# Kernel tuning notes

Measured on AMD Instinct MI355X. Metric: run time of the kernel, lower is better.

## Reference

```python
import jax, jax.numpy as jnp
import numpy as np

GAMMA = 5.0 / 3.0
N, H = 131072, 256


def mlp(c, W1, b1, W2, b2, W3, b3, W4, b4):
    h = jnp.tanh(c @ W1 + b1)
    h = jnp.tanh(h @ W2 + b2)
    h = jnp.tanh(h @ W3 + b3)
    return h @ W4 + b4  # [N, 6] -> (rho, vx, vy, Bx, By, P)


def setup_inputs() -> dict:
    key = jax.random.key(0)
    ks = jax.random.split(key, 6)
    s = 0.5
    return {
        "coords": jax.random.uniform(ks[0], (N, 3), jnp.float32),  # (x, y, t)
        "W1": jax.random.normal(ks[1], (3, H), jnp.float32) * s,
        "b1": jnp.zeros((H,), jnp.float32),
        "W2": jax.random.normal(ks[2], (H, H), jnp.float32) * (s / np.sqrt(H)),
        "b2": jnp.zeros((H,), jnp.float32),
        "W3": jax.random.normal(ks[3], (H, H), jnp.float32) * (s / np.sqrt(H)),
        "b3": jnp.zeros((H,), jnp.float32),
        "W4": jax.random.normal(ks[4], (H, 6), jnp.float32) * (s / np.sqrt(H)),
        "b4": jnp.zeros((6,), jnp.float32),
        "weights": jnp.ones((7,), jnp.float32),
    }


def reference(coords, W1, b1, W2, b2, W3, b3, W4, b4, weights):
    f = lambda c: mlp(c, W1, b1, W2, b2, W3, b3, W4, b4)
    preds = f(coords)
    # Batched Jacobian d preds / d coords via 3 forward-mode JVPs (basis dirs x,y,t)
    eye = jnp.eye(3, dtype=coords.dtype)
    jvp1 = lambda e: jax.jvp(f, (coords,), (jnp.broadcast_to(e, coords.shape),))[1]
    J = jnp.transpose(jax.vmap(jvp1)(eye), (1, 2, 0))  # [N, 6, 3]

    rho, vx, vy, Bx, By, P = (preds[:, k] for k in range(6))
    Jx, Jy, Jt = J[..., 0], J[..., 1], J[..., 2]  # each [N, 6]

    # time derivatives (chain rule for composite fields)
    dt_rho = Jt[:, 0]
    dt_Bx, dt_By = Jt[:, 3], Jt[:, 4]
    dt_rhovx = dt_rho * vx + rho * Jt[:, 1]
    dt_rhovy = dt_rho * vy + rho * Jt[:, 2]

    def dE(Jc):  # derivative of total energy E along coord c
        return (Jc[:, 5] / (GAMMA - 1.0)
                + 0.5 * Jc[:, 0] * (vx ** 2 + vy ** 2)
                + rho * (vx * Jc[:, 1] + vy * Jc[:, 2])
                + Bx * Jc[:, 3] + By * Jc[:, 4])

    dE_dx, dE_dy, dE_dt = dE(Jx), dE(Jy), dE(Jt)

    div_v = Jx[:, 1] + Jy[:, 2]
    div_B = Jx[:, 3] + Jy[:, 4]
    continuity = dt_rho + rho * div_v

    # grad of total pressure P + 0.5*(Bx^2 + By^2)
    dPm_dx = Jx[:, 5] + Bx * Jx[:, 3] + By * Jx[:, 4]
    dPm_dy = Jy[:, 5] + Bx * Jy[:, 3] + By * Jy[:, 4]
    momentum_x = dt_rhovx + dPm_dx - (Bx * Jx[:, 3] + By * Jy[:, 3])
    momentum_y = dt_rhovy + dPm_dy - (Bx * Jx[:, 4] + By * Jy[:, 4])

    # induction: G = vx*By - vy*Bx
    def dG(Jc):
        return Jc[:, 1] * By + vx * Jc[:, 4] - Jc[:, 2] * Bx - vy * Jc[:, 3]

    induction_x = dt_Bx + dG(Jy)
    induction_y = dt_By - dG(Jx)

    # energy: d/dt E + div( S*v - D*B ), S = E + P + Pm, D = B.v
    E = P / (GAMMA - 1.0) + 0.5 * rho * (vx ** 2 + vy ** 2) + 0.5 * (Bx ** 2 + By ** 2)
    S = E + P + 0.5 * (Bx ** 2 + By ** 2)
    dS_dx = dE_dx + Jx[:, 5] + Bx * Jx[:, 3] + By * Jx[:, 4]
    dS_dy = dE_dy + Jy[:, 5] + Bx * Jy[:, 3] + By * Jy[:, 4]
    D = Bx * vx + By * vy

    def dD(Jc):
        return Jc[:, 3] * vx + Bx * Jc[:, 1] + Jc[:, 4] * vy + By * Jc[:, 2]

    dFx_dx = dS_dx * vx + S * Jx[:, 1] - dD(Jx) * Bx - D * Jx[:, 3]
    dFy_dy = dS_dy * vy + S * Jy[:, 2] - dD(Jy) * By - D * Jy[:, 4]
    energy = dE_dt + dFx_dx + dFy_dy

    res = [continuity, momentum_x, momentum_y, induction_x, induction_y, energy, div_B]
    loss = sum(w * jnp.mean(r ** 2) for w, r in zip(weights, res))
    return loss
```

## Files before the change

kernel.cpp:

```cpp
#include <hip/hip_runtime.h>
#include <hip/hip_bf16.h>
#include <cstdint>


#define LDW 264
#define TPTS 16
#define GRIDB 256

typedef __attribute__((ext_vector_type(8))) short v8h;
typedef __attribute__((ext_vector_type(4))) float v4f;

__device__ __forceinline__ ushort f2b(float f) {
    uint32_t u = __float_as_uint(f);
    u = (u + 0x7fffu + ((u >> 16) & 1u)) >> 16;
    return (ushort)u;
}
__device__ __forceinline__ uint32_t pk2(float a, float b) {
    union { __hip_bfloat162 h2; uint32_t u; } cv;
    cv.h2 = __float22bfloat162_rn(make_float2(a, b));
    return cv.u;
}
__device__ __forceinline__ float fast_tanh(float x) {
    float e = __expf(2.0f * x);
    return 1.0f - 2.0f * __builtin_amdgcn_rcpf(e + 1.0f);
}

__global__ void prep_weights(const float* __restrict__ W2, const float* __restrict__ W3,
                             const float* __restrict__ W4,
                             ushort* __restrict__ Wt2, ushort* __restrict__ Wt3,
                             ushort* __restrict__ Wt4) {
    int idx = blockIdx.x * 256 + threadIdx.x;
    if (idx < 65536) {
        int k = idx >> 8, n = idx & 255;
        Wt2[n * 256 + k] = f2b(W2[k * 256 + n]);
        Wt3[n * 256 + k] = f2b(W3[k * 256 + n]);
    }
    if (idx < 4096) {
        int n = idx >> 8, k = idx & 255;
        Wt4[n * 256 + k] = (n < 6) ? f2b(W4[k * 6 + n]) : (ushort)0;
    }
}

__device__ __forceinline__ void dense_layer(const ushort* __restrict__ src,
                                            ushort* __restrict__ dst,
                                            const v8h (*wf)[8], const v4f* bs,
                                            int wv, int q, int l15) {
    v4f acc[2][4];
    #pragma unroll
    for (int a = 0; a < 2; a++)
        #pragma unroll
        for (int b = 0; b < 4; b++) {
            v4f z = {0.0f, 0.0f, 0.0f, 0.0f};
            acc[a][b] = z;
        }
    #pragma unroll
    for (int kk = 0; kk < 8; kk++) {
        v8h B[4];
        #pragma unroll
        for (int nt = 0; nt < 4; nt++)
            B[nt] = *(const v8h*)(&src[(nt * 16 + l15) * LDW + kk * 32 + q * 8]);
        #pragma unroll
        for (int mt = 0; mt < 2; mt++)
            #pragma unroll
            for (int nt = 0; nt < 4; nt++)
                acc[mt][nt] = __builtin_amdgcn_mfma_f32_16x16x32_bf16(wf[mt][kk], B[nt], acc[mt][nt], 0, 0, 0);
    }
    #pragma unroll
    for (int mt = 0; mt < 2; mt++) {
        const int colb = wv * 32 + mt * 16 + q * 4;
        v4f bb = bs[mt];
        float h0 = fast_tanh(acc[mt][0][0] + bb[0]);
        float h1 = fast_tanh(acc[mt][0][1] + bb[1]);
        float h2 = fast_tanh(acc[mt][0][2] + bb[2]);
        float h3 = fast_tanh(acc[mt][0][3] + bb[3]);
        float d0 = 1.0f - h0 * h0, d1 = 1.0f - h1 * h1;
        float d2 = 1.0f - h2 * h2, d3 = 1.0f - h3 * h3;
        uint2 w;
        w.x = pk2(h0, h1); w.y = pk2(h2, h3);
        *(uint2*)(&dst[l15 * LDW + colb]) = w;
        #pragma unroll
        for (int s = 1; s < 4; s++) {
            w.x = pk2(d0 * acc[mt][s][0], d1 * acc[mt][s][1]);
            w.y = pk2(d2 * acc[mt][s][2], d3 * acc[mt][s][3]);
            *(uint2*)(&dst[(s * 16 + l15) * LDW + colb]) = w;
        }
    }
}

__global__ __launch_bounds__(512, 2)
void mhd_fused(const float* __restrict__ coords,
               const float* __restrict__ W1, const float* __restrict__ b1,
               const float* __restrict__ b2, const float* __restrict__ b3,
               const float* __restrict__ b4,
               const float* __restrict__ wts,
               const ushort* __restrict__ Wt2, const ushort* __restrict__ Wt3,
               const ushort* __restrict__ Wt4,
               float* __restrict__ out, int npts, float inv_n) {
    __shared__ ushort Xs0[64 * LDW];
    __shared__ ushort Xs1[64 * LDW];
    __shared__ ushort W4s[16 * LDW];
    __shared__ float  cs[TPTS * 3];
    __shared__ float  Y4[4][TPTS][8];

    const int tid  = threadIdx.x;
    const int lane = tid & 63;
    const int wv   = tid >> 6;
    const int q    = lane >> 4;
    const int l15  = lane & 15;

    for (int idx = tid; idx < 16 * 256; idx += 512)
        W4s[(idx >> 8) * LDW + (idx & 255)] = Wt4[idx];

    v8h w2f[2][8], w3f[2][8];
    v4f bs2[2], bs3[2];
    #pragma unroll
    for (int mt = 0; mt < 2; mt++) {
        const int nrow = (wv * 32 + mt * 16 + l15) * 256 + q * 8;
        #pragma unroll
        for (int kk = 0; kk < 8; kk++) {
            w2f[mt][kk] = *(const v8h*)(&Wt2[nrow + kk * 32]);
            w3f[mt][kk] = *(const v8h*)(&Wt3[nrow + kk * 32]);
        }
        bs2[mt] = *(const v4f*)(&b2[wv * 32 + mt * 16 + q * 4]);
        bs3[mt] = *(const v4f*)(&b3[wv * 32 + mt * 16 + q * 4]);
    }

    const int jj = tid & 255, ph = tid >> 8;
    const float l1w0 = W1[jj], l1w1 = W1[256 + jj], l1w2 = W1[512 + jj], l1b = b1[jj];
    const float b40 = b4[0], b41 = b4[1], b42 = b4[2], b43 = b4[3], b44 = b4[4], b45 = b4[5];
    const float wt0 = wts[0], wt1 = wts[1], wt2_ = wts[2], wt3_ = wts[3],
                wt4_ = wts[4], wt5 = wts[5], wt6 = wts[6];

    const int ntiles = (npts + TPTS - 1) / TPTS;
    float vsum = 0.0f;

    for (int tile = blockIdx.x; tile < ntiles; tile += GRIDB) {
        const int base = tile * TPTS;

        if (tid < TPTS * 3) {
            int p = tid / 3, c = tid % 3;
            int gp = base + p; if (gp >= npts) gp = npts - 1;
            cs[tid] = coords[gp * 3 + c];
        }
        __syncthreads();

        #pragma unroll
        for (int pp = 0; pp < 8; pp++) {
            const int p = ph * 8 + pp;
            float x = cs[p * 3], y = cs[p * 3 + 1], t = cs[p * 3 + 2];
            float pre = fmaf(x, l1w0, fmaf(y, l1w1, fmaf(t, l1w2, l1b)));
            float h = fast_tanh(pre);
            float d = 1.0f - h * h;
            Xs0[p * LDW + jj]        = f2b(h);
            Xs0[(16 + p) * LDW + jj] = f2b(d * l1w0);
            Xs0[(32 + p) * LDW + jj] = f2b(d * l1w1);
            Xs0[(48 + p) * LDW + jj] = f2b(d * l1w2);
        }
        __syncthreads();

        dense_layer(Xs0, Xs1, w2f, bs2, wv, q, l15);
        __syncthreads();
        dense_layer(Xs1, Xs0, w3f, bs3, wv, q, l15);
        __syncthreads();

        if (wv < 4) {
            v4f a4 = {0.0f, 0.0f, 0.0f, 0.0f};
            #pragma unroll
            for (int kk = 0; kk < 8; kk++) {
                v8h A = *(const v8h*)(&W4s[l15 * LDW + kk * 32 + q * 8]);
                v8h B = *(const v8h*)(&Xs0[(wv * 16 + l15) * LDW + kk * 32 + q * 8]);
                a4 = __builtin_amdgcn_mfma_f32_16x16x32_bf16(A, B, a4, 0, 0, 0);
            }
            if (q < 2) {
                #pragma unroll
                for (int r = 0; r < 4; r++)
                    Y4[wv][l15][q * 4 + r] = a4[r];
            }
        }
        __syncthreads();

        if (tid < 16 && (base + tid) < npts) {
            const float* Yh = Y4[0][tid];
            const float* JX = Y4[1][tid];
            const float* JY = Y4[2][tid];
            const float* JT = Y4[3][tid];
            const float g1 = 1.5f;
            float rho = Yh[0] + b40, vx = Yh[1] + b41, vy = Yh[2] + b42;
            float Bx  = Yh[3] + b43, By = Yh[4] + b44, P  = Yh[5] + b45;
            float v2 = vx * vx + vy * vy;
            float dt_rho = JT[0];
            float dt_rhovx = dt_rho * vx + rho * JT[1];
            float dt_rhovy = dt_rho * vy + rho * JT[2];
            auto dE = [&](const float* J) {
                return J[5] * g1 + 0.5f * J[0] * v2 + rho * (vx * J[1] + vy * J[2]) + Bx * J[3] + By * J[4];
            };
            float dE_dx = dE(JX), dE_dy = dE(JY), dE_dt = dE(JT);
            float div_v = JX[1] + JY[2];
            float div_B = JX[3] + JY[4];
            float continuity = dt_rho + rho * div_v;
            float dPm_dx = JX[5] + Bx * JX[3] + By * JX[4];
            float dPm_dy = JY[5] + Bx * JY[3] + By * JY[4];
            float momentum_x = dt_rhovx + dPm_dx - (Bx * JX[3] + By * JY[3]);
            float momentum_y = dt_rhovy + dPm_dy - (Bx * JX[4] + By * JY[4]);
            auto dG = [&](const float* J) {
                return J[1] * By + vx * J[4] - J[2] * Bx - vy * J[3];
            };
            float induction_x = JT[3] + dG(JY);
            float induction_y = JT[4] - dG(JX);
            float E = P * g1 + 0.5f * rho * v2 + 0.5f * (Bx * Bx + By * By);
            float S = E + P + 0.5f * (Bx * Bx + By * By);
            float dS_dx = dE_dx + JX[5] + Bx * JX[3] + By * JX[4];
            float dS_dy = dE_dy + JY[5] + Bx * JY[3] + By * JY[4];
            float D = Bx * vx + By * vy;
            auto dD = [&](const float* J) {
                return J[3] * vx + Bx * J[1] + J[4] * vy + By * J[2];
            };
            float dFx_dx = dS_dx * vx + S * JX[1] - dD(JX) * Bx - D * JX[3];
            float dFy_dy = dS_dy * vy + S * JY[2] - dD(JY) * By - D * JY[4];
            float energy = dE_dt + dFx_dx + dFy_dy;
            vsum += wt0 * continuity * continuity
                  + wt1 * momentum_x * momentum_x
                  + wt2_ * momentum_y * momentum_y
                  + wt3_ * induction_x * induction_x
                  + wt4_ * induction_y * induction_y
                  + wt5 * energy * energy
                  + wt6 * div_B * div_B;
        }
    }

    if (tid < 64) {
        #pragma unroll
        for (int off = 8; off >= 1; off >>= 1)
            vsum += __shfl_down(vsum, off, 64);
        if (tid == 0) atomicAdd(out, vsum * inv_n);
    }
}

extern "C" void kernel_launch(void* const* d_in, const int* in_sizes, int n_in,
                              void* d_out, int out_size, void* d_ws, size_t ws_size,
                              hipStream_t stream) {
    const float* coords = (const float*)d_in[0];
    const float* W1 = (const float*)d_in[1];
    const float* b1 = (const float*)d_in[2];
    const float* W2 = (const float*)d_in[3];
    const float* b2 = (const float*)d_in[4];
    const float* W3 = (const float*)d_in[5];
    const float* b3 = (const float*)d_in[6];
    const float* W4 = (const float*)d_in[7];
    const float* b4 = (const float*)d_in[8];
    const float* wts = (const float*)d_in[9];
    const int npts = in_sizes[0] / 3;

    ushort* Wt2 = (ushort*)d_ws;
    ushort* Wt3 = Wt2 + 65536;
    ushort* Wt4 = Wt3 + 65536;

    hipMemsetAsync(d_out, 0, sizeof(float), stream);
    prep_weights<<<256, 256, 0, stream>>>(W2, W3, W4, Wt2, Wt3, Wt4);
    mhd_fused<<<GRIDB, 512, 0, stream>>>(coords, W1, b1, b2, b3, b4, wts,
                                         Wt2, Wt3, Wt4, (float*)d_out, npts, 1.0f / npts);
}
```

Measured before the change: 247.8 us.

## Software-pipeline layer-1 and residual across tiles with XOR-swizzled LDS

Replaces the padded LDS layout with an XOR-swizzled 512-byte row layout to avoid bank conflicts, and double-buffers the layer-1 input so the next tile's first layer is computed before the current tile's dense layers. The residual evaluation is deferred by two iterations into a double-buffered Y4, run by wave 7 while other work proceeds, which drops one barrier per tile. Layer 1 now reads coords directly from global memory and writes 4 columns per thread as vector stores. LDS use grows (an extra input buffer), which may limit occupancy at two blocks per CU.

Result: slower. 322.1 us (+30.0%).

```diff
diff --git a/kernel.cpp b/kernel.cpp
--- a/kernel.cpp
+++ b/kernel.cpp
@@ -3,9 +3,8 @@
 #include <cstdint>
 
 
-#define LDW 264
+#define GRIDB 256
 #define TPTS 16
-#define GRIDB 256
 
 typedef __attribute__((ext_vector_type(8))) short v8h;
 typedef __attribute__((ext_vector_type(4))) float v4f;
@@ -23,6 +22,9 @@
 __device__ __forceinline__ float fast_tanh(float x) {
     float e = __expf(2.0f * x);
     return 1.0f - 2.0f * __builtin_amdgcn_rcpf(e + 1.0f);
+}
+__device__ __forceinline__ int swz(int row, int bytecol) {
+    return (row << 9) + ((((bytecol >> 4) ^ (row & 31)) << 4) | (bytecol & 15));
 }
 
 __global__ void prep_weights(const float* __restrict__ W2, const float* __restrict__ W3,
@@ -41,52 +43,6 @@
     }
 }
 
-__device__ __forceinline__ void dense_layer(const ushort* __restrict__ src,
-                                            ushort* __restrict__ dst,
-                                            const v8h (*wf)[8], const v4f* bs,
-                                            int wv, int q, int l15) {
-    v4f acc[2][4];
-    #pragma unroll
-    for (int a = 0; a < 2; a++)
-        #pragma unroll
-        for (int b = 0; b < 4; b++) {
-            v4f z = {0.0f, 0.0f, 0.0f, 0.0f};
-            acc[a][b] = z;
-        }
-    #pragma unroll
-    for (int kk = 0; kk < 8; kk++) {
-        v8h B[4];
-        #pragma unroll
-        for (int nt = 0; nt < 4; nt++)
-            B[nt] = *(const v8h*)(&src[(nt * 16 + l15) * LDW + kk * 32 + q * 8]);
-        #pragma unroll
-        for (int mt = 0; mt < 2; mt++)
-            #pragma unroll
-            for (int nt = 0; nt < 4; nt++)
-                acc[mt][nt] = __builtin_amdgcn_mfma_f32_16x16x32_bf16(wf[mt][kk], B[nt], acc[mt][nt], 0, 0, 0);
-    }
-    #pragma unroll
-    for (int mt = 0; mt < 2; mt++) {
-        const int colb = wv * 32 + mt * 16 + q * 4;
-        v4f bb = bs[mt];
-        float h0 = fast_tanh(acc[mt][0][0] + bb[0]);
-        float h1 = fast_tanh(acc[mt][0][1] + bb[1]);
-        float h2 = fast_tanh(acc[mt][0][2] + bb[2]);
-        float h3 = fast_tanh(acc[mt][0][3] + bb[3]);
-        float d0 = 1.0f - h0 * h0, d1 = 1.0f - h1 * h1;
-        float d2 = 1.0f - h2 * h2, d3 = 1.0f - h3 * h3;
-        uint2 w;
-        w.x = pk2(h0, h1); w.y = pk2(h2, h3);
-        *(uint2*)(&dst[l15 * LDW + colb]) = w;
-        #pragma unroll
-        for (int s = 1; s < 4; s++) {
-            w.x = pk2(d0 * acc[mt][s][0], d1 * acc[mt][s][1]);
-            w.y = pk2(d2 * acc[mt][s][2], d3 * acc[mt][s][3]);
-            *(uint2*)(&dst[(s * 16 + l15) * LDW + colb]) = w;
-        }
-    }
-}
-
 __global__ __launch_bounds__(512, 2)
 void mhd_fused(const float* __restrict__ coords,
                const float* __restrict__ W1, const float* __restrict__ b1,
@@ -96,11 +52,11 @@
                const ushort* __restrict__ Wt2, const ushort* __restrict__ Wt3,
                const ushort* __restrict__ Wt4,
                float* __restrict__ out, int npts, float inv_n) {
-    __shared__ ushort Xs0[64 * LDW];
-    __shared__ ushort Xs1[64 * LDW];
-    __shared__ ushort W4s[16 * LDW];
-    __shared__ float  cs[TPTS * 3];
-    __shared__ float  Y4[4][TPTS][8];
+    __shared__ __align__(16) uint8_t XinB[2][64 * 512];
+    __shared__ __align__(16) uint8_t Xmid[64 * 512];
+    __shared__ __align__(16) uint8_t Xout[64 * 512];
+    __shared__ __align__(16) uint8_t W4s[16 * 512];
+    __shared__ float Y4[2][4][TPTS][8];
 
     const int tid  = threadIdx.x;
     const int lane = tid & 63;
@@ -108,8 +64,11 @@
     const int q    = lane >> 4;
     const int l15  = lane & 15;
 
-    for (int idx = tid; idx < 16 * 256; idx += 512)
-        W4s[(idx >> 8) * LDW + (idx & 255)] = Wt4[idx];
+    for (int idx = tid; idx < 16 * 128; idx += 512) {
+        int n = idx >> 7, kdw = idx & 127;
+        *(uint32_t*)(&W4s[(n << 9) + ((((kdw >> 2) ^ n) << 4) | ((kdw & 3) << 2))]) =
+            ((const uint32_t*)Wt4)[idx];
+    }
 
     v8h w2f[2][8], w3f[2][8];
     v4f bs2[2], bs3[2];
@@ -125,114 +84,184 @@
         bs3[mt] = *(const v4f*)(&b3[wv * 32 + mt * 16 + q * 4]);
     }
 
-    const int jj = tid & 255, ph = tid >> 8;
-    const float l1w0 = W1[jj], l1w1 = W1[256 + jj], l1w2 = W1[512 + jj], l1b = b1[jj];
+    const int j0 = (tid & 63) * 4, pg = tid >> 6;
+    float l1w0[4], l1w1[4], l1w2[4], l1b[4];
+    #pragma unroll
+    for (int c = 0; c < 4; c++) {
+        l1w0[c] = W1[j0 + c]; l1w1[c] = W1[256 + j0 + c];
+        l1w2[c] = W1[512 + j0 + c]; l1b[c] = b1[j0 + c];
+    }
+
     const float b40 = b4[0], b41 = b4[1], b42 = b4[2], b43 = b4[3], b44 = b4[4], b45 = b4[5];
     const float wt0 = wts[0], wt1 = wts[1], wt2_ = wts[2], wt3_ = wts[3],
                 wt4_ = wts[4], wt5 = wts[5], wt6 = wts[6];
 
+    auto do_l1 = [&](int tile, uint8_t* Xin) {
+        const int base = tile * TPTS;
+        #pragma unroll
+        for (int pp = 0; pp < 2; pp++) {
+            const int p = pg * 2 + pp;
+            int gp = base + p; if (gp >= npts) gp = npts - 1;
+            float x = coords[gp * 3], y = coords[gp * 3 + 1], t = coords[gp * 3 + 2];
+            float h[4], d[4];
+            #pragma unroll
+            for (int c = 0; c < 4; c++) {
+                h[c] = fast_tanh(fmaf(x, l1w0[c], fmaf(y, l1w1[c], fmaf(t, l1w2[c], l1b[c]))));
+                d[c] = 1.0f - h[c] * h[c];
+            }
+            uint2 w;
+            const int bc = j0 * 2;
+            w.x = pk2(h[0], h[1]); w.y = pk2(h[2], h[3]);
+            *(uint2*)(&Xin[swz(p, bc)]) = w;
+            w.x = pk2(d[0] * l1w0[0], d[1] * l1w0[1]); w.y = pk2(d[2] * l1w0[2], d[3] * l1w0[3]);
+            *(uint2*)(&Xin[swz(16 + p, bc)]) = w;
+            w.x = pk2(d[0] * l1w1[0], d[1] * l1w1[1]); w.y = pk2(d[2] * l1w1[2], d[3] * l1w1[3]);
+            *(uint2*)(&Xin[swz(32 + p, bc)]) = w;
+            w.x = pk2(d[0] * l1w2[0], d[1] * l1w2[1]); w.y = pk2(d[2] * l1w2[2], d[3] * l1w2[3]);
+            *(uint2*)(&Xin[swz(48 + p, bc)]) = w;
+        }
+    };
+
+    auto dense = [&](const uint8_t* src, uint8_t* dst, const v8h (*wf)[8], const v4f* bs) {
+        v4f acc[2][4];
+        #pragma unroll
+        for (int a = 0; a < 2; a++)
+            #pragma unroll
+            for (int b = 0; b < 4; b++) {
+                v4f z = {0.0f, 0.0f, 0.0f, 0.0f};
+                acc[a][b] = z;
+            }
+        #pragma unroll
+        for (int kk = 0; kk < 8; kk++) {
+            v8h B[4];
+            #pragma unroll
+            for (int nt = 0; nt < 4; nt++) {
+                const int row = nt * 16 + l15;
+                B[nt] = *(const v8h*)(&src[(row << 9) + ((((kk * 4 + q) ^ (row & 31)) << 4))]);
+            }
+            #pragma unroll
+            for (int mt = 0; mt < 2; mt++)
+                #pragma unroll
+                for (int nt = 0; nt < 4; nt++)
+                    acc[mt][nt] = __builtin_amdgcn_mfma_f32_16x16x32_bf16(wf[mt][kk], B[nt], acc[mt][nt], 0, 0, 0);
+        }
+        #pragma unroll
+        for (int mt = 0; mt < 2; mt++) {
+            const int bc = wv * 64 + mt * 32 + q * 8;
+            v4f bb = bs[mt];
+            float h0 = fast_tanh(acc[mt][0][0] + bb[0]);
+            float h1 = fast_tanh(acc[mt][0][1] + bb[1]);
+            float h2 = fast_tanh(acc[mt][0][2] + bb[2]);
+            float h3 = fast_tanh(acc[mt][0][3] + bb[3]);
+            float d0 = 1.0f - h0 * h0, d1 = 1.0f - h1 * h1;
+            float d2 = 1.0f - h2 * h2, d3 = 1.0f - h3 * h3;
+            uint2 w;
+            w.x = pk2(h0, h1); w.y = pk2(h2, h3);
+            *(uint2*)(&dst[swz(l15, bc)]) = w;
+            #pragma unroll
+            for (int s = 1; s < 4; s++) {
+                w.x = pk2(d0 * acc[mt][s][0], d1 * acc[mt][s][1]);
+                w.y = pk2(d2 * acc[mt][s][2], d3 * acc[mt][s][3]);
+                *(uint2*)(&dst[swz(s * 16 + l15, bc)]) = w;
+            }
+        }
+    };
+
+    auto residual = [&](int tile, int par) -> float {
+        const int gp = tile * TPTS + lane;
+        if (gp >= npts) return 0.0f;
+        const float* Yh = Y4[par][0][lane];
+        const float* JX = Y4[par][1][lane];
+        const float* JY = Y4[par][2][lane];
+        const float* JT = Y4[par][3][lane];
+        const float g1 = 1.5f;
+        float rho = Yh[0] + b40, vx = Yh[1] + b41, vy = Yh[2] + b42;
+        float Bx  = Yh[3] + b43, By = Yh[4] + b44, P  = Yh[5] + b45;
+        float v2 = vx * vx + vy * vy;
+        float dt_rho = JT[0];
+        float dt_rhovx = dt_rho * vx + rho * JT[1];
+        float dt_rhovy = dt_rho * vy + rho * JT[2];
+        auto dE = [&](const float* J) {
+            return J[5] * g1 + 0.5f * J[0] * v2 + rho * (vx * J[1] + vy * J[2]) + Bx * J[3] + By * J[4];
+        };
+        float dE_dx = dE(JX), dE_dy = dE(JY), dE_dt = dE(JT);
+        float div_v = JX[1] + JY[2];
+        float div_B = JX[3] + JY[4];
+        float continuity = dt_rho + rho * div_v;
+        float dPm_dx = JX[5] + Bx * JX[3] + By * JX[4];
+        float dPm_dy = JY[5] + Bx * JY[3] + By * JY[4];
+        float momentum_x = dt_rhovx + dPm_dx - (Bx * JX[3] + By * JY[3]);
+        float momentum_y = dt_rhovy + dPm_dy - (Bx * JX[4] + By * JY[4]);
+        auto dG = [&](const float* J) {
+            return J[1] * By + vx * J[4] - J[2] * Bx - vy * J[3];
+        };
+        float induction_x = JT[3] + dG(JY);
+        float induction_y = JT[4] - dG(JX);
+        float E = P * g1 + 0.5f * rho * v2 + 0.5f * (Bx * Bx + By * By);
+        float S = E + P + 0.5f * (Bx * Bx + By * By);
+        float dS_dx = dE_dx + JX[5] + Bx * JX[3] + By * JX[4];
+        float dS_dy = dE_dy + JY[5] + Bx * JY[3] + By * JY[4];
+        float D = Bx * vx + By * vy;
+        auto dD = [&](const float* J) {
+            return J[3] * vx + Bx * J[1] + J[4] * vy + By * J[2];
+        };
+        float dFx_dx = dS_dx * vx + S * JX[1] - dD(JX) * Bx - D * JX[3];
+        float dFy_dy = dS_dy * vy + S * JY[2] - dD(JY) * By - D * JY[4];
+        float energy = dE_dt + dFx_dx + dFy_dy;
+        return wt0 * continuity * continuity
+             + wt1 * momentum_x * momentum_x
+             + wt2_ * momentum_y * momentum_y
+             + wt3_ * induction_x * induction_x
+             + wt4_ * induction_y * induction_y
+             + wt5 * energy * energy
+             + wt6 * div_B * div_B;
+    };
+
     const int ntiles = (npts + TPTS - 1) / TPTS;
+    const int myblk  = blockIdx.x;
+    const int nit    = (myblk < ntiles) ? ((ntiles - 1 - myblk) / GRIDB + 1) : 0;
     float vsum = 0.0f;
 
-    for (int tile = blockIdx.x; tile < ntiles; tile += GRIDB) {
-        const int base = tile * TPTS;
-
-        if (tid < TPTS * 3) {
-            int p = tid / 3, c = tid % 3;
-            int gp = base + p; if (gp >= npts) gp = npts - 1;
-            cs[tid] = coords[gp * 3 + c];
-        }
+    if (nit > 0) do_l1(myblk, XinB[0]);
+
+    for (int i = 0; i < nit; i++) {
+        const int tile = myblk + i * GRIDB;
+        if (wv == 7 && lane < TPTS && i >= 2)
+            vsum += residual(tile - 2 * GRIDB, i & 1);
+        if (i + 1 < nit) do_l1(tile + GRIDB, XinB[(i + 1) & 1]);
         __syncthreads();
-
-        #pragma unroll
-        for (int pp = 0; pp < 8; pp++) {
-            const int p = ph * 8 + pp;
-            float x = cs[p * 3], y = cs[p * 3 + 1], t = cs[p * 3 + 2];
-            float pre = fmaf(x, l1w0, fmaf(y, l1w1, fmaf(t, l1w2, l1b)));
-            float h = fast_tanh(pre);
-            float d = 1.0f - h * h;
-            Xs0[p * LDW + jj]        = f2b(h);
-            Xs0[(16 + p) * LDW + jj] = f2b(d * l1w0);
-            Xs0[(32 + p) * LDW + jj] = f2b(d * l1w1);
-            Xs0[(48 + p) * LDW + jj] = f2b(d * l1w2);
-        }
+        dense(XinB[i & 1], Xmid, w2f, bs2);
         __syncthreads();
-
-        dense_layer(Xs0, Xs1, w2f, bs2, wv, q, l15);
+        dense(Xmid, Xout, w3f, bs3);
         __syncthreads();
-        dense_layer(Xs1, Xs0, w3f, bs3, wv, q, l15);
-        __syncthreads();
-
         if (wv < 4) {
             v4f a4 = {0.0f, 0.0f, 0.0f, 0.0f};
             #pragma unroll
             for (int kk = 0; kk < 8; kk++) {
-                v8h A = *(const v8h*)(&W4s[l15 * LDW + kk * 32 + q * 8]);
-                v8h B = *(const v8h*)(&Xs0[(wv * 16 + l15) * LDW + kk * 32 + q * 8]);
+                v8h A = *(const v8h*)(&W4s[(l15 << 9) + (((kk * 4 + q) ^ l15) << 4)]);
+                const int rowB = wv * 16 + l15;
+                v8h B = *(const v8h*)(&Xout[(rowB << 9) + ((((kk * 4 + q) ^ (rowB & 31)) << 4))]);
                 a4 = __builtin_amdgcn_mfma_f32_16x16x32_bf16(A, B, a4, 0, 0, 0);
             }
             if (q < 2) {
                 #pragma unroll
                 for (int r = 0; r < 4; r++)
-                    Y4[wv][l15][q * 4 + r] = a4[r];
-            }
-        }
-        __syncthreads();
-
-        if (tid < 16 && (base + tid) < npts) {
-            const float* Yh = Y4[0][tid];
-            const float* JX = Y4[1][tid];
-            const float* JY = Y4[2][tid];
-            const float* JT = Y4[3][tid];
-            const float g1 = 1.5f;
-            float rho = Yh[0] + b40, vx = Yh[1] + b41, vy = Yh[2] + b42;
-            float Bx  = Yh[3] + b43, By = Yh[4] + b44, P  = Yh[5] + b45;
-            float v2 = vx * vx + vy * vy;
-            float dt_rho = JT[0];
-            float dt_rhovx = dt_rho * vx + rho * JT[1];
-            float dt_rhovy = dt_rho * vy + rho * JT[2];
-            auto dE = [&](const float* J) {
-                return J[5] * g1 + 0.5f * J[0] * v2 + rho * (vx * J[1] + vy * J[2]) + Bx * J[3] + By * J[4];
-            };
-            float dE_dx = dE(JX), dE_dy = dE(JY), dE_dt = dE(JT);
-            float div_v = JX[1] + JY[2];
-            float div_B = JX[3] + JY[4];
-            float continuity = dt_rho + rho * div_v;
-            float dPm_dx = JX[5] + Bx * JX[3] + By * JX[4];
-            float dPm_dy = JY[5] + Bx * JY[3] + By * JY[4];
-            float momentum_x = dt_rhovx + dPm_dx - (Bx * JX[3] + By * JY[3]);
-            float momentum_y = dt_rhovy + dPm_dy - (Bx * JX[4] + By * JY[4]);
-            auto dG = [&](const float* J) {
-                return J[1] * By + vx * J[4] - J[2] * Bx - vy * J[3];
-            };
-            float induction_x = JT[3] + dG(JY);
-            float induction_y = JT[4] - dG(JX);
-            float E = P * g1 + 0.5f * rho * v2 + 0.5f * (Bx * Bx + By * By);
-            float S = E + P + 0.5f * (Bx * Bx + By * By);
-            float dS_dx = dE_dx + JX[5] + Bx * JX[3] + By * JX[4];
-            float dS_dy = dE_dy + JY[5] + Bx * JY[3] + By * JY[4];
-            float D = Bx * vx + By * vy;
-            auto dD = [&](const float* J) {
-                return J[3] * vx + Bx * J[1] + J[4] * vy + By * J[2];
-            };
-            float dFx_dx = dS_dx * vx + S * JX[1] - dD(JX) * Bx - D * JX[3];
-            float dFy_dy = dS_dy * vy + S * JY[2] - dD(JY) * By - D * JY[4];
-            float energy = dE_dt + dFx_dx + dFy_dy;
-            vsum += wt0 * continuity * continuity
-                  + wt1 * momentum_x * momentum_x
-                  + wt2_ * momentum_y * momentum_y
-                  + wt3_ * induction_x * induction_x
-                  + wt4_ * induction_y * induction_y
-                  + wt5 * energy * energy
-                  + wt6 * div_B * div_B;
-        }
-    }
-
-    if (tid < 64) {
+                    Y4[i & 1][wv][l15][q * 4 + r] = a4[r];
+            }
+        }
+    }
+
+    __syncthreads();
+    if (wv == 7 && lane < TPTS) {
+        if (nit >= 2) vsum += residual(myblk + (nit - 2) * GRIDB, nit & 1);
+        if (nit >= 1) vsum += residual(myblk + (nit - 1) * GRIDB, (nit - 1) & 1);
+    }
+
+    if (wv == 7) {
         #pragma unroll
         for (int off = 8; off >= 1; off >>= 1)
             vsum += __shfl_down(vsum, off, 64);
-        if (tid == 0) atomicAdd(out, vsum * inv_n);
+        if (lane == 0) atomicAdd(out, vsum * inv_n);
     }
 }
 
@@ -255,7 +284,7 @@
     ushort* Wt3 = Wt2 + 65536;
     ushort* Wt4 = Wt3 + 65536;
 
-    hipMemsetAsync(d_out, 0, sizeof(float), stream);
+    (void)hipMemsetAsync(d_out, 0, sizeof(float), stream);
     prep_weights<<<256, 256, 0, stream>>>(W2, W3, W4, Wt2, Wt3, Wt4);
     mhd_fused<<<GRIDB, 512, 0, stream>>>(coords, W1, b1, b2, b3, b4, wts,
                                          Wt2, Wt3, Wt4, (float*)d_out, npts, 1.0f / npts);
```
